# Performance work log

Measured on AMD Instinct MI355X. Metric: run time of the kernel, lower is better.

## Reference

```python
import jax, jax.numpy as jnp
import numpy as np

T = 19          # TIME_STEPS from the source
N = 20000
EMB = 64        # embedding_dim
HID = 128       # hidden_dim
SCALE = 4.0     # InputEmbedding scale
ENC_STEPS = 8   # LRP code: encoder weights for t < 8, decoder after


def setup_inputs():
    key = jax.random.key(0)
    ks = jax.random.split(key, 16)
    obs = jax.random.normal(ks[0], (T, N, 2), dtype=jnp.float32) * 5.0
    # tracks appear at random start times -> NaN before start (drives track_mask)
    starts = jax.random.randint(ks[1], (N,), 0, 10)
    active = jnp.arange(T)[:, None] >= starts[None, :]
    obs = jnp.where(active[:, :, None], obs, jnp.nan)
    goals = jax.random.normal(ks[2], (N, 2), dtype=jnp.float32)

    def p(k, shape):
        return jax.random.normal(k, shape, dtype=jnp.float32) * 0.05

    return {
        "obs": obs, "goals": goals,
        "w_emb": p(ks[3], (EMB, 2)), "b_emb": p(ks[4], (EMB,)),
        "w_ih_e": p(ks[5], (4 * HID, EMB)), "b_ih_e": p(ks[6], (4 * HID,)),
        "w_hh_e": p(ks[7], (4 * HID, HID)), "b_hh_e": p(ks[8], (4 * HID,)),
        "w_ih_d": p(ks[9], (4 * HID, EMB)), "b_ih_d": p(ks[10], (4 * HID,)),
        "w_hh_d": p(ks[11], (4 * HID, HID)), "b_hh_d": p(ks[12], (4 * HID,)),
        "w_out": p(ks[13], (5, HID)), "b_out": p(ks[14], (5,)),
    }


def _lstm_cell(x, h, c, w_ih, b_ih, w_hh, b_hh):
    # torch.nn.LSTMCell: gate order i, f, g, o
    gates = x @ w_ih.T + b_ih + h @ w_hh.T + b_hh  # [n, 4H]
    i, f, g, o = jnp.split(gates, 4, axis=-1)
    i, f, o = jax.nn.sigmoid(i), jax.nn.sigmoid(f), jax.nn.sigmoid(o)
    g = jnp.tanh(g)
    c2 = f * c + i * g
    h2 = o * jnp.tanh(c2)
    return h2, c2


def _hidden2normal(h, w_out, b_out):
    n = h @ w_out.T + b_out  # [n, 5]
    return jnp.concatenate([
        n[:, :2],
        0.01 + 0.2 * jax.nn.sigmoid(n[:, 2:4]),  # sigmas
        0.7 * jax.nn.sigmoid(n[:, 4:5]),          # rho
    ], axis=1)


def _run_steps(obs1_seq, obs2_seq, h, c, w_emb, b_emb, w_ih, b_ih, w_hh, b_hh, w_out, b_out):
    def step(carry, ob):
        h, c = carry
        o1, o2 = ob
        # track_mask: active iff neither position is NaN (masked gather in torch)
        mask = ~(jnp.isnan(o1[:, 0]) | jnp.isnan(o2[:, 0]))
        m = mask[:, None]
        vel = jnp.where(m, o2 - o1, 0.0)                      # sanitize NaNs
        emb = jax.nn.relu((vel * SCALE) @ w_emb.T + b_emb)    # InputEmbedding
        h2, c2 = _lstm_cell(emb, h, c, w_ih, b_ih, w_hh, b_hh)
        normal = jnp.where(m, _hidden2normal(h2, w_out, b_out), 0.0)
        # scatter updated state back only for active tracks
        return (jnp.where(m, h2, h), jnp.where(m, c2, c)), normal

    (h, c), normals = jax.lax.scan(step, (h, c), (obs1_seq, obs2_seq))
    return h, c, normals


def reference(obs, goals, w_emb, b_emb, w_ih_e, b_ih_e, w_hh_e, b_hh_e,
              w_ih_d, b_ih_d, w_hh_d, b_hh_d, w_out, b_out):
    del goals  # goal_flag=False: goal embedding branch disabled
    n = obs.shape[1]
    h = jnp.zeros((n, HID), dtype=obs.dtype)
    c = jnp.zeros((n, HID), dtype=obs.dtype)
    o1, o2 = obs[:-1], obs[1:]
    h, c, n_enc = _run_steps(o1[:ENC_STEPS], o2[:ENC_STEPS], h, c,
                             w_emb, b_emb, w_ih_e, b_ih_e, w_hh_e, b_hh_e, w_out, b_out)
    h, c, n_dec = _run_steps(o1[ENC_STEPS:], o2[ENC_STEPS:], h, c,
                             w_emb, b_emb, w_ih_d, b_ih_d, w_hh_d, b_hh_d, w_out, b_out)
    return jnp.concatenate([n_enc, n_dec], axis=0)  # [T-1, N, 5]
```

## Files before the change

### kernel.cpp

```cpp
#include <hip/hip_runtime.h>

#define T_OUT 18
#define NAG   20000
#define EMBD  64
#define HIDD  128
#define APB   80
#define SH    136
#define SE    72

typedef _Float16 half8 __attribute__((ext_vector_type(8)));
typedef float    f32x4 __attribute__((ext_vector_type(4)));

__device__ __forceinline__ float rcpf(float x) { return __builtin_amdgcn_rcpf(x); }
__device__ __forceinline__ float sigmf(float x) { return rcpf(1.0f + __expf(-x)); }

__global__ __launch_bounds__(512, 2)
void lstm_seq_kernel(
    const float* __restrict__ obs,
    const float* __restrict__ w_emb,  const float* __restrict__ b_emb,
    const float* __restrict__ w_ih_e, const float* __restrict__ b_ih_e,
    const float* __restrict__ w_hh_e, const float* __restrict__ b_hh_e,
    const float* __restrict__ w_ih_d, const float* __restrict__ b_ih_d,
    const float* __restrict__ w_hh_d, const float* __restrict__ b_hh_d,
    const float* __restrict__ w_out,  const float* __restrict__ b_out,
    float* __restrict__ out)
{
  __shared__ __align__(16) _Float16 h_s[2][APB * SH];
  __shared__ __align__(16) _Float16 e_s[2][APB * SE];
  __shared__ float vel_s[2][APB * 2];
  __shared__ float mask_s[4][APB];

  const int tid = threadIdx.x;
  const int wv  = tid >> 6;
  const int ln  = tid & 63;
  const int l15 = ln & 15;
  const int lg  = ln >> 4;
  const int a0  = blockIdx.x * APB;
  const int po  = tid - 320;
  const bool obsOwner = ((unsigned)po) < APB;
  const float2* obs2 = (const float2*)obs;

  for (int i = tid; i < APB * SH; i += 512) h_s[0][i] = (_Float16)0.f;

  const float we0 = 4.f * w_emb[ln * 2 + 0];
  const float we1 = 4.f * w_emb[ln * 2 + 1];
  const float be  = b_emb[ln];

  float oAx = 0.f, oAy = 0.f;
  if (obsOwner) {
    int a = a0 + po;
    float2 o0 = obs2[0 * NAG + a];
    float2 o1 = obs2[1 * NAG + a];
    float2 o2 = obs2[2 * NAG + a];
    bool k0 = !__builtin_isnan(o0.x) && !__builtin_isnan(o1.x);
    bool k1 = !__builtin_isnan(o1.x) && !__builtin_isnan(o2.x);
    mask_s[0][po] = k0 ? 1.f : 0.f;
    vel_s[0][po * 2 + 0] = k0 ? (o1.x - o0.x) : 0.f;
    vel_s[0][po * 2 + 1] = k0 ? (o1.y - o0.y) : 0.f;
    mask_s[1][po] = k1 ? 1.f : 0.f;
    vel_s[1][po * 2 + 0] = k1 ? (o2.x - o1.x) : 0.f;
    vel_s[1][po * 2 + 1] = k1 ? (o2.y - o1.y) : 0.f;
    oAx = o2.x; oAy = o2.y;
  }

  half8 fih[4][2];
  half8 fhh[4][4];
  half8 fout[4];
  float bsum[4], bo;

  {
    int j = l15;
    #pragma unroll
    for (int ks = 0; ks < 4; ks++) {
      half8 v;
      #pragma unroll
      for (int q = 0; q < 8; q++) {
        float x = (j < 5) ? w_out[j * HIDD + ks * 32 + lg * 8 + q] : 0.f;
        v[q] = (_Float16)x;
      }
      fout[ks] = v;
    }
    bo = (j < 5) ? b_out[j] : 0.f;
  }

  auto load_phase = [&](const float* wih, const float* bih,
                        const float* whh, const float* bhh) {
    #pragma unroll
    for (int n = 0; n < 4; n++) {
      int row = n * 128 + wv * 16 + l15;
      #pragma unroll
      for (int ks = 0; ks < 2; ks++) {
        const float* p = wih + row * EMBD + ks * 32 + lg * 8;
        half8 v;
        #pragma unroll
        for (int q = 0; q < 8; q++) v[q] = (_Float16)p[q];
        fih[n][ks] = v;
      }
      #pragma unroll
      for (int ks = 0; ks < 4; ks++) {
        const float* p = whh + row * HIDD + ks * 32 + lg * 8;
        half8 v;
        #pragma unroll
        for (int q = 0; q < 8; q++) v[q] = (_Float16)p[q];
        fhh[n][ks] = v;
      }
      bsum[n] = bih[row] + bhh[row];
    }
  };

  auto emb_compute = [&](int ebuf, int vbuf) {
    #pragma unroll
    for (int k = 0; k < 10; k++) {
      int a = wv + 8 * k;
      float vx = vel_s[vbuf][a * 2], vy = vel_s[vbuf][a * 2 + 1];
      float e = fmaf(vx, we0, fmaf(vy, we1, be));
      e_s[ebuf][a * SE + ln] = (_Float16)fmaxf(e, 0.f);
    }
  };

  load_phase(w_ih_e, b_ih_e, w_hh_e, b_hh_e);
  __syncthreads();
  emb_compute(0, 0);
  __syncthreads();

  float c_r[5][4];
  float h_r[5][4];
  #pragma unroll
  for (int m = 0; m < 5; m++)
    #pragma unroll
    for (int r = 0; r < 4; r++) { c_r[m][r] = 0.f; h_r[m][r] = 0.f; }

  const int hid = wv * 16 + l15;

  #pragma unroll 1
  for (int t = 0; t < T_OUT; t++) {
    if (t == 8) load_phase(w_ih_d, b_ih_d, w_hh_d, b_hh_d);

    const int idx  = t & 1;
    const int nidx = idx ^ 1;
    const int msC  = t & 3;
    const int msP  = (t + 3) & 3;

    float n3x = 0.f, n3y = 0.f;
    if (t + 2 < T_OUT && obsOwner) {
      float2 o = obs2[(size_t)(t + 3) * NAG + a0 + po];
      n3x = o.x; n3y = o.y;
    }

    #pragma unroll
    for (int m = 0; m < 5; m++) {
      f32x4 acc[4];
      #pragma unroll
      for (int n = 0; n < 4; n++)
        acc[n] = f32x4{bsum[n], bsum[n], bsum[n], bsum[n]};

      #pragma unroll
      for (int ks = 0; ks < 2; ks++) {
        half8 av = *(const half8*)&e_s[idx][(m * 16 + l15) * SE + ks * 32 + lg * 8];
        #pragma unroll
        for (int n = 0; n < 4; n++)
          acc[n] = __builtin_amdgcn_mfma_f32_16x16x32_f16(av, fih[n][ks], acc[n], 0, 0, 0);
      }
      #pragma unroll
      for (int ks = 0; ks < 4; ks++) {
        half8 av = *(const half8*)&h_s[idx][(m * 16 + l15) * SH + ks * 32 + lg * 8];
        #pragma unroll
        for (int n = 0; n < 4; n++)
          acc[n] = __builtin_amdgcn_mfma_f32_16x16x32_f16(av, fhh[n][ks], acc[n], 0, 0, 0);
      }

      float c2a[4], ova[4];
      #pragma unroll
      for (int r = 0; r < 4; r++) {
        float ai = acc[0][r], af = acc[1][r];
        float ag_ = acc[2][r], ao = acc[3][r];
        float ei = __expf(-ai), ef = __expf(-af);
        float eo = __expf(-ao), eg = __expf(-2.f * ag_);
        float di = 1.f + ei, df = 1.f + ef, dd = 1.f + eo, dg = 1.f + eg;
        float p1 = rcpf(di * df);
        float iv = df * p1, fv = di * p1;
        float p2 = rcpf(dd * dg);
        float ov = dg * p2;
        float gv = fmaf(2.f, dd * p2, -1.f);
        c2a[r] = fmaf(fv, c_r[m][r], iv * gv);
        ova[r] = ov;
      }
      float dc[4];
      #pragma unroll
      for (int r = 0; r < 4; r++) dc[r] = 1.f + __expf(-2.f * c2a[r]);
      float q01 = rcpf(dc[0] * dc[1]);
      float q23 = rcpf(dc[2] * dc[3]);
      float inv[4] = { dc[1] * q01, dc[0] * q01, dc[3] * q23, dc[2] * q23 };
      #pragma unroll
      for (int r = 0; r < 4; r++) {
        int ag = m * 16 + lg * 4 + r;
        float mk = mask_s[msC][ag];
        float th = fmaf(2.f, inv[r], -1.f);
        float h2 = ova[r] * th;
        bool on = (mk != 0.f);
        c_r[m][r] = on ? c2a[r] : c_r[m][r];
        _Float16 hh = (_Float16)(on ? h2 : h_r[m][r]);
        h_s[nidx][ag * SH + hid] = hh;
        h_r[m][r] = (float)hh;
      }
    }

    if (t > 0 && wv < 5) {
      f32x4 oa = f32x4{bo, bo, bo, bo};
      #pragma unroll
      for (int ks = 0; ks < 4; ks++) {
        half8 av = *(const half8*)&h_s[idx][(wv * 16 + l15) * SH + ks * 32 + lg * 8];
        oa = __builtin_amdgcn_mfma_f32_16x16x32_f16(av, fout[ks], oa, 0, 0, 0);
      }
      int j = l15;
      #pragma unroll
      for (int r = 0; r < 4; r++) {
        int ag = wv * 16 + lg * 4 + r;
        float mk = mask_s[msP][ag];
        float nv = oa[r];
        float y;
        if (j < 2)      y = nv;
        else if (j < 4) y = 0.01f + 0.2f * sigmf(nv);
        else            y = 0.7f * sigmf(nv);
        if (j < 5) out[((size_t)(t - 1) * NAG + a0 + ag) * 5 + j] = y * mk;
      }
    }

    if (t + 1 < T_OUT) emb_compute(nidx, (t + 1) & 1);

    if (t + 2 < T_OUT && obsOwner) {
      bool ok = !__builtin_isnan(oAx) && !__builtin_isnan(n3x);
      mask_s[(t + 2) & 3][po] = ok ? 1.f : 0.f;
      vel_s[t & 1][po * 2 + 0] = ok ? (n3x - oAx) : 0.f;
      vel_s[t & 1][po * 2 + 1] = ok ? (n3y - oAy) : 0.f;
      oAx = n3x; oAy = n3y;
    }

    __syncthreads();
  }

  if (wv < 5) {
    f32x4 oa = f32x4{bo, bo, bo, bo};
    #pragma unroll
    for (int ks = 0; ks < 4; ks++) {
      half8 av = *(const half8*)&h_s[T_OUT & 1][(wv * 16 + l15) * SH + ks * 32 + lg * 8];
      oa = __builtin_amdgcn_mfma_f32_16x16x32_f16(av, fout[ks], oa, 0, 0, 0);
    }
    int j = l15;
    #pragma unroll
    for (int r = 0; r < 4; r++) {
      int ag = wv * 16 + lg * 4 + r;
      float mk = mask_s[(T_OUT - 1) & 3][ag];
      float nv = oa[r];
      float y;
      if (j < 2)      y = nv;
      else if (j < 4) y = 0.01f + 0.2f * sigmf(nv);
      else            y = 0.7f * sigmf(nv);
      if (j < 5) out[((size_t)(T_OUT - 1) * NAG + a0 + ag) * 5 + j] = y * mk;
    }
  }
}

extern "C" void kernel_launch(void* const* d_in, const int* in_sizes, int n_in,
                              void* d_out, int out_size, void* d_ws, size_t ws_size,
                              hipStream_t stream) {
  const float* obs    = (const float*)d_in[0];
  const float* w_emb  = (const float*)d_in[2];
  const float* b_emb  = (const float*)d_in[3];
  const float* w_ih_e = (const float*)d_in[4];
  const float* b_ih_e = (const float*)d_in[5];
  const float* w_hh_e = (const float*)d_in[6];
  const float* b_hh_e = (const float*)d_in[7];
  const float* w_ih_d = (const float*)d_in[8];
  const float* b_ih_d = (const float*)d_in[9];
  const float* w_hh_d = (const float*)d_in[10];
  const float* b_hh_d = (const float*)d_in[11];
  const float* w_out  = (const float*)d_in[12];
  const float* b_out  = (const float*)d_in[13];
  float* out = (float*)d_out;

  lstm_seq_kernel<<<dim3(250), dim3(512), 0, stream>>>(
      obs, w_emb, b_emb, w_ih_e, b_ih_e, w_hh_e, b_hh_e,
      w_ih_d, b_ih_d, w_hh_d, b_hh_d, w_out, b_out, out);
}
```

Baseline: 134.6 us.

## Split LSTM gates across 16 waves and combine cell update via LDS

Doubles the block to 1024 threads. Each wave now computes two 16-column tiles of one gate type (i, f, g or o) with MFMA and applies that gate's activation. The activated gates go to a new fp16 LDS buffer, and a second elementwise phase, after an extra barrier, reads all four gates per hidden unit and updates c and h. The aim is to double active waves per CU, since only about one block runs per CU, and to spread the transcendental work. The cost is an extra barrier per timestep, about 83KB more LDS traffic, and rounding gate activations to fp16.

```diff
diff --git a/kernel.cpp b/kernel.cpp
--- a/kernel.cpp
+++ b/kernel.cpp
@@ -7,14 +7,17 @@
 #define APB   80
 #define SH    136
 #define SE    72
+#define SG    520
 
 typedef _Float16 half8 __attribute__((ext_vector_type(8)));
+typedef _Float16 half4 __attribute__((ext_vector_type(4)));
 typedef float    f32x4 __attribute__((ext_vector_type(4)));
 
 __device__ __forceinline__ float rcpf(float x) { return __builtin_amdgcn_rcpf(x); }
 __device__ __forceinline__ float sigmf(float x) { return rcpf(1.0f + __expf(-x)); }
 
-__global__ __launch_bounds__(512, 2)
+__global__
+__attribute__((amdgpu_flat_work_group_size(1024, 1024)))
 void lstm_seq_kernel(
     const float* __restrict__ obs,
     const float* __restrict__ w_emb,  const float* __restrict__ b_emb,
@@ -26,47 +29,48 @@
     float* __restrict__ out)
 {
   __shared__ __align__(16) _Float16 h_s[2][APB * SH];
-  __shared__ __align__(16) _Float16 e_s[2][APB * SE];
+  __shared__ __align__(16) _Float16 e_s[APB * SE];
+  __shared__ __align__(16) _Float16 g_s[APB * SG];
   __shared__ float vel_s[2][APB * 2];
   __shared__ float mask_s[4][APB];
 
-  const int tid = threadIdx.x;
-  const int wv  = tid >> 6;
-  const int ln  = tid & 63;
-  const int l15 = ln & 15;
-  const int lg  = ln >> 4;
-  const int a0  = blockIdx.x * APB;
-  const int po  = tid - 320;
-  const bool obsOwner = ((unsigned)po) < APB;
+  const int tid  = threadIdx.x;
+  const int wv   = tid >> 6;
+  const int ln   = tid & 63;
+  const int l15  = ln & 15;
+  const int lg   = ln >> 4;
+  const int a0   = blockIdx.x * APB;
+  const int gate = wv >> 2;
+  const int hcB  = (wv & 3) * 32;
   const float2* obs2 = (const float2*)obs;
 
-  for (int i = tid; i < APB * SH; i += 512) h_s[0][i] = (_Float16)0.f;
+  for (int i = tid; i < APB * SH; i += 1024) h_s[0][i] = (_Float16)0.f;
 
   const float we0 = 4.f * w_emb[ln * 2 + 0];
   const float we1 = 4.f * w_emb[ln * 2 + 1];
   const float be  = b_emb[ln];
 
   float oAx = 0.f, oAy = 0.f;
-  if (obsOwner) {
-    int a = a0 + po;
+  if (tid < APB) {
+    int a = a0 + tid;
     float2 o0 = obs2[0 * NAG + a];
     float2 o1 = obs2[1 * NAG + a];
     float2 o2 = obs2[2 * NAG + a];
     bool k0 = !__builtin_isnan(o0.x) && !__builtin_isnan(o1.x);
     bool k1 = !__builtin_isnan(o1.x) && !__builtin_isnan(o2.x);
-    mask_s[0][po] = k0 ? 1.f : 0.f;
-    vel_s[0][po * 2 + 0] = k0 ? (o1.x - o0.x) : 0.f;
-    vel_s[0][po * 2 + 1] = k0 ? (o1.y - o0.y) : 0.f;
-    mask_s[1][po] = k1 ? 1.f : 0.f;
-    vel_s[1][po * 2 + 0] = k1 ? (o2.x - o1.x) : 0.f;
-    vel_s[1][po * 2 + 1] = k1 ? (o2.y - o1.y) : 0.f;
+    mask_s[0][tid] = k0 ? 1.f : 0.f;
+    vel_s[0][tid * 2 + 0] = k0 ? (o1.x - o0.x) : 0.f;
+    vel_s[0][tid * 2 + 1] = k0 ? (o1.y - o0.y) : 0.f;
+    mask_s[1][tid] = k1 ? 1.f : 0.f;
+    vel_s[1][tid * 2 + 0] = k1 ? (o2.x - o1.x) : 0.f;
+    vel_s[1][tid * 2 + 1] = k1 ? (o2.y - o1.y) : 0.f;
     oAx = o2.x; oAy = o2.y;
   }
 
-  half8 fih[4][2];
-  half8 fhh[4][4];
+  half8 fih[2][2];
+  half8 fhh[2][4];
   half8 fout[4];
-  float bsum[4], bo;
+  float bsum[2], bo;
 
   {
     int j = l15;
@@ -86,15 +90,15 @@
   auto load_phase = [&](const float* wih, const float* bih,
                         const float* whh, const float* bhh) {
     #pragma unroll
-    for (int n = 0; n < 4; n++) {
-      int row = n * 128 + wv * 16 + l15;
+    for (int tile = 0; tile < 2; tile++) {
+      int row = wv * 32 + tile * 16 + l15;
       #pragma unroll
       for (int ks = 0; ks < 2; ks++) {
         const float* p = wih + row * EMBD + ks * 32 + lg * 8;
         half8 v;
         #pragma unroll
         for (int q = 0; q < 8; q++) v[q] = (_Float16)p[q];
-        fih[n][ks] = v;
+        fih[tile][ks] = v;
       }
       #pragma unroll
       for (int ks = 0; ks < 4; ks++) {
@@ -102,35 +106,33 @@
         half8 v;
         #pragma unroll
         for (int q = 0; q < 8; q++) v[q] = (_Float16)p[q];
-        fhh[n][ks] = v;
-      }
-      bsum[n] = bih[row] + bhh[row];
+        fhh[tile][ks] = v;
+      }
+      bsum[tile] = bih[row] + bhh[row];
     }
   };
 
-  auto emb_compute = [&](int ebuf, int vbuf) {
-    #pragma unroll
-    for (int k = 0; k < 10; k++) {
-      int a = wv + 8 * k;
-      float vx = vel_s[vbuf][a * 2], vy = vel_s[vbuf][a * 2 + 1];
+  auto emb_compute = [&](int vb) {
+    #pragma unroll
+    for (int k = 0; k < 5; k++) {
+      int a = wv + 16 * k;
+      float vx = vel_s[vb][a * 2], vy = vel_s[vb][a * 2 + 1];
       float e = fmaf(vx, we0, fmaf(vy, we1, be));
-      e_s[ebuf][a * SE + ln] = (_Float16)fmaxf(e, 0.f);
+      e_s[a * SE + ln] = (_Float16)fmaxf(e, 0.f);
     }
   };
 
   load_phase(w_ih_e, b_ih_e, w_hh_e, b_hh_e);
   __syncthreads();
-  emb_compute(0, 0);
+  emb_compute(0);
   __syncthreads();
 
-  float c_r[5][4];
-  float h_r[5][4];
+  float c_r[10];
   #pragma unroll
-  for (int m = 0; m < 5; m++)
-    #pragma unroll
-    for (int r = 0; r < 4; r++) { c_r[m][r] = 0.f; h_r[m][r] = 0.f; }
-
-  const int hid = wv * 16 + l15;
+  for (int k = 0; k < 10; k++) c_r[k] = 0.f;
+
+  const int aBase = tid >> 7;
+  const int hc    = tid & 127;
 
   #pragma unroll 1
   for (int t = 0; t < T_OUT; t++) {
@@ -142,121 +144,130 @@
     const int msP  = (t + 3) & 3;
 
     float n3x = 0.f, n3y = 0.f;
-    if (t + 2 < T_OUT && obsOwner) {
-      float2 o = obs2[(size_t)(t + 3) * NAG + a0 + po];
+    if (t + 2 < T_OUT && tid < APB) {
+      float2 o = obs2[(size_t)(t + 3) * NAG + a0 + tid];
       n3x = o.x; n3y = o.y;
     }
 
     #pragma unroll
     for (int m = 0; m < 5; m++) {
-      f32x4 acc[4];
-      #pragma unroll
-      for (int n = 0; n < 4; n++)
-        acc[n] = f32x4{bsum[n], bsum[n], bsum[n], bsum[n]};
-
+      f32x4 A0 = f32x4{bsum[0], bsum[0], bsum[0], bsum[0]};
+      f32x4 A1 = f32x4{bsum[1], bsum[1], bsum[1], bsum[1]};
       #pragma unroll
       for (int ks = 0; ks < 2; ks++) {
-        half8 av = *(const half8*)&e_s[idx][(m * 16 + l15) * SE + ks * 32 + lg * 8];
-        #pragma unroll
-        for (int n = 0; n < 4; n++)
-          acc[n] = __builtin_amdgcn_mfma_f32_16x16x32_f16(av, fih[n][ks], acc[n], 0, 0, 0);
+        half8 av = *(const half8*)&e_s[(m * 16 + l15) * SE + ks * 32 + lg * 8];
+        A0 = __builtin_amdgcn_mfma_f32_16x16x32_f16(av, fih[0][ks], A0, 0, 0, 0);
+        A1 = __builtin_amdgcn_mfma_f32_16x16x32_f16(av, fih[1][ks], A1, 0, 0, 0);
       }
       #pragma unroll
       for (int ks = 0; ks < 4; ks++) {
         half8 av = *(const half8*)&h_s[idx][(m * 16 + l15) * SH + ks * 32 + lg * 8];
-        #pragma unroll
-        for (int n = 0; n < 4; n++)
-          acc[n] = __builtin_amdgcn_mfma_f32_16x16x32_f16(av, fhh[n][ks], acc[n], 0, 0, 0);
-      }
-
-      float c2a[4], ova[4];
+        A0 = __builtin_amdgcn_mfma_f32_16x16x32_f16(av, fhh[0][ks], A0, 0, 0, 0);
+        A1 = __builtin_amdgcn_mfma_f32_16x16x32_f16(av, fhh[1][ks], A1, 0, 0, 0);
+      }
+
+      float v[8] = {A0[0], A0[1], A0[2], A0[3], A1[0], A1[1], A1[2], A1[3]};
+      float r[8];
+      if (gate == 2) {
+        float d[8];
+        #pragma unroll
+        for (int i = 0; i < 8; i++) d[i] = 1.f + __expf(-2.f * v[i]);
+        #pragma unroll
+        for (int i = 0; i < 8; i += 2) {
+          float p = rcpf(d[i] * d[i + 1]);
+          r[i]     = fmaf(2.f, d[i + 1] * p, -1.f);
+          r[i + 1] = fmaf(2.f, d[i] * p, -1.f);
+        }
+      } else {
+        float d[8];
+        #pragma unroll
+        for (int i = 0; i < 8; i++) d[i] = 1.f + __expf(-v[i]);
+        #pragma unroll
+        for (int i = 0; i < 8; i += 2) {
+          float p = rcpf(d[i] * d[i + 1]);
+          r[i]     = d[i + 1] * p;
+          r[i + 1] = d[i] * p;
+        }
+      }
+      #pragma unroll
+      for (int i = 0; i < 8; i++) {
+        int agent = m * 16 + lg * 4 + (i & 3);
+        int hcw   = hcB + (i >> 2) * 16 + l15;
+        g_s[agent * SG + hcw * 4 + gate] = (_Float16)r[i];
+      }
+    }
+
+    if (t > 0 && wv >= 11) {
+      int mo = wv - 11;
+      f32x4 oa = f32x4{bo, bo, bo, bo};
+      #pragma unroll
+      for (int ks = 0; ks < 4; ks++) {
+        half8 av = *(const half8*)&h_s[idx][(mo * 16 + l15) * SH + ks * 32 + lg * 8];
+        oa = __builtin_amdgcn_mfma_f32_16x16x32_f16(av, fout[ks], oa, 0, 0, 0);
+      }
+      int j = l15;
       #pragma unroll
       for (int r = 0; r < 4; r++) {
-        float ai = acc[0][r], af = acc[1][r];
-        float ag_ = acc[2][r], ao = acc[3][r];
-        float ei = __expf(-ai), ef = __expf(-af);
-        float eo = __expf(-ao), eg = __expf(-2.f * ag_);
-        float di = 1.f + ei, df = 1.f + ef, dd = 1.f + eo, dg = 1.f + eg;
-        float p1 = rcpf(di * df);
-        float iv = df * p1, fv = di * p1;
-        float p2 = rcpf(dd * dg);
-        float ov = dg * p2;
-        float gv = fmaf(2.f, dd * p2, -1.f);
-        c2a[r] = fmaf(fv, c_r[m][r], iv * gv);
-        ova[r] = ov;
-      }
-      float dc[4];
-      #pragma unroll
-      for (int r = 0; r < 4; r++) dc[r] = 1.f + __expf(-2.f * c2a[r]);
-      float q01 = rcpf(dc[0] * dc[1]);
-      float q23 = rcpf(dc[2] * dc[3]);
-      float inv[4] = { dc[1] * q01, dc[0] * q01, dc[3] * q23, dc[2] * q23 };
-      #pragma unroll
-      for (int r = 0; r < 4; r++) {
-        int ag = m * 16 + lg * 4 + r;
-        float mk = mask_s[msC][ag];
-        float th = fmaf(2.f, inv[r], -1.f);
-        float h2 = ova[r] * th;
-        bool on = (mk != 0.f);
-        c_r[m][r] = on ? c2a[r] : c_r[m][r];
-        _Float16 hh = (_Float16)(on ? h2 : h_r[m][r]);
-        h_s[nidx][ag * SH + hid] = hh;
-        h_r[m][r] = (float)hh;
-      }
-    }
-
-    if (t > 0 && wv < 5) {
-      f32x4 oa = f32x4{bo, bo, bo, bo};
-      #pragma unroll
-      for (int ks = 0; ks < 4; ks++) {
-        half8 av = *(const half8*)&h_s[idx][(wv * 16 + l15) * SH + ks * 32 + lg * 8];
-        oa = __builtin_amdgcn_mfma_f32_16x16x32_f16(av, fout[ks], oa, 0, 0, 0);
-      }
-      int j = l15;
-      #pragma unroll
-      for (int r = 0; r < 4; r++) {
-        int ag = wv * 16 + lg * 4 + r;
-        float mk = mask_s[msP][ag];
+        int agent = mo * 16 + lg * 4 + r;
+        float mk = mask_s[msP][agent];
         float nv = oa[r];
         float y;
         if (j < 2)      y = nv;
         else if (j < 4) y = 0.01f + 0.2f * sigmf(nv);
         else            y = 0.7f * sigmf(nv);
-        if (j < 5) out[((size_t)(t - 1) * NAG + a0 + ag) * 5 + j] = y * mk;
-      }
-    }
-
-    if (t + 1 < T_OUT) emb_compute(nidx, (t + 1) & 1);
-
-    if (t + 2 < T_OUT && obsOwner) {
+        if (j < 5) out[((size_t)(t - 1) * NAG + a0 + agent) * 5 + j] = y * mk;
+      }
+    }
+
+    __syncthreads();
+
+    #pragma unroll
+    for (int k = 0; k < 10; k++) {
+      int a = aBase + 8 * k;
+      half4 g4 = *(const half4*)&g_s[a * SG + hc * 4];
+      float iv = (float)g4[0], fv = (float)g4[1];
+      float gv = (float)g4[2], ov = (float)g4[3];
+      float c2 = fmaf(fv, c_r[k], iv * gv);
+      float th = fmaf(2.f, rcpf(1.f + __expf(-2.f * c2)), -1.f);
+      float mk = mask_s[msC][a];
+      bool on = (mk != 0.f);
+      c_r[k] = on ? c2 : c_r[k];
+      _Float16 hold = h_s[idx][a * SH + hc];
+      h_s[nidx][a * SH + hc] = on ? (_Float16)(ov * th) : hold;
+    }
+
+    if (t + 1 < T_OUT) emb_compute((t + 1) & 1);
+
+    if (t + 2 < T_OUT && tid < APB) {
       bool ok = !__builtin_isnan(oAx) && !__builtin_isnan(n3x);
-      mask_s[(t + 2) & 3][po] = ok ? 1.f : 0.f;
-      vel_s[t & 1][po * 2 + 0] = ok ? (n3x - oAx) : 0.f;
-      vel_s[t & 1][po * 2 + 1] = ok ? (n3y - oAy) : 0.f;
+      mask_s[(t + 2) & 3][tid] = ok ? 1.f : 0.f;
+      vel_s[t & 1][tid * 2 + 0] = ok ? (n3x - oAx) : 0.f;
+      vel_s[t & 1][tid * 2 + 1] = ok ? (n3y - oAy) : 0.f;
       oAx = n3x; oAy = n3y;
     }
 
     __syncthreads();
   }
 
-  if (wv < 5) {
+  if (wv >= 11) {
+    int mo = wv - 11;
     f32x4 oa = f32x4{bo, bo, bo, bo};
     #pragma unroll
     for (int ks = 0; ks < 4; ks++) {
-      half8 av = *(const half8*)&h_s[T_OUT & 1][(wv * 16 + l15) * SH + ks * 32 + lg * 8];
+      half8 av = *(const half8*)&h_s[T_OUT & 1][(mo * 16 + l15) * SH + ks * 32 + lg * 8];
       oa = __builtin_amdgcn_mfma_f32_16x16x32_f16(av, fout[ks], oa, 0, 0, 0);
     }
     int j = l15;
     #pragma unroll
     for (int r = 0; r < 4; r++) {
-      int ag = wv * 16 + lg * 4 + r;
-      float mk = mask_s[(T_OUT - 1) & 3][ag];
+      int agent = mo * 16 + lg * 4 + r;
+      float mk = mask_s[(T_OUT - 1) & 3][agent];
       float nv = oa[r];
       float y;
       if (j < 2)      y = nv;
       else if (j < 4) y = 0.01f + 0.2f * sigmf(nv);
       else            y = 0.7f * sigmf(nv);
-      if (j < 5) out[((size_t)(T_OUT - 1) * NAG + a0 + ag) * 5 + j] = y * mk;
+      if (j < 5) out[((size_t)(T_OUT - 1) * NAG + a0 + agent) * 5 + j] = y * mk;
     }
   }
 }
@@ -279,7 +290,7 @@
   const float* b_out  = (const float*)d_in[13];
   float* out = (float*)d_out;
 
-  lstm_seq_kernel<<<dim3(250), dim3(512), 0, stream>>>(
+  lstm_seq_kernel<<<dim3(250), dim3(1024), 0, stream>>>(
       obs, w_emb, b_emb, w_ih_e, b_ih_e, w_hh_e, b_hh_e,
       w_ih_d, b_ih_d, w_hh_d, b_hh_d, w_out, b_out, out);
 }
```

New measurement: 178.9 us. 32.9% more time.
